# Optimization experiments

Measured on AMD Instinct MI355X. Metric: run time of the kernel, lower is better.

Reference implementation:

```python
import jax, jax.numpy as jnp
import numpy as np

NUM_HEADS = 8  # from init_kwargs
SR = 2         # sr_ratio from init_kwargs


def layernorm(t, g, b, eps=1e-5):
    mu = jnp.mean(t, axis=-1, keepdims=True)
    var = jnp.mean((t - mu) ** 2, axis=-1, keepdims=True)
    return (t - mu) * jax.lax.rsqrt(var + eps) * g + b


def setup_inputs() -> dict:
    key = jax.random.key(0)
    ks = jax.random.split(key, 6)
    B, C = 4, 256
    Hx = Wx = 64
    Hz = Wz = 32
    N = Hz * Wz + Hx * Wx  # 5120 (template tokens first, then search tokens)
    s = 0.02
    return {
        "x": jax.random.normal(ks[0], (B, N, C), jnp.float32),
        "Wq": jax.random.normal(ks[1], (C, C), jnp.float32) * s,          # nn.Linear(dim, dim, bias=False)
        "Wkv": jax.random.normal(ks[2], (2 * C, C), jnp.float32) * s,     # nn.Linear(dim, 2*dim, bias=False)
        "Wsr": jax.random.normal(ks[3], (C, C, SR, SR), jnp.float32) * s, # Conv2d(dim, dim, k=sr, stride=sr) OIHW
        "bsr": jnp.zeros((C,), jnp.float32),
        "gamma": jnp.ones((C,), jnp.float32),
        "beta": jnp.zeros((C,), jnp.float32),
        "Wproj": jax.random.normal(ks[4], (C, C), jnp.float32) * s,
        "bproj": jnp.zeros((C,), jnp.float32),
        "H_x": Hx, "W_x": Wx, "H_z": Hz, "W_z": Wz,
    }


def reference(x, Wq, Wkv, Wsr, bsr, gamma, beta, Wproj, bproj, H_x, W_x, H_z, W_z):
    B, N, C = x.shape
    h = NUM_HEADS
    d = C // h
    scale = d ** -0.5
    Nz, Nx = H_z * W_z, H_x * W_x

    # q for all tokens: [B, h, N, d]
    q = (x @ Wq.T).reshape(B, N, h, d).transpose(0, 2, 1, 3)

    # spatial reduction (sr_ratio > 1 branch): strided conv + layernorm on each stream
    z_tok, x_tok = x[:, :Nz], x[:, Nz:]
    ker = jnp.transpose(Wsr, (2, 3, 1, 0))  # OIHW -> HWIO

    def sr_branch(t, H, W):
        img = t.reshape(B, H, W, C)  # NHWC; same layout as torch NCHW reshape
        out = jax.lax.conv_general_dilated(
            img, ker, window_strides=(SR, SR), padding="VALID",
            dimension_numbers=("NHWC", "HWIO", "NHWC")) + bsr
        out = out.reshape(B, -1, C)
        return layernorm(out, gamma, beta)

    x_ = sr_branch(x_tok, H_x, W_x)  # [B, (Hx/sr)*(Wx/sr), C]
    z_ = sr_branch(z_tok, H_z, W_z)  # [B, (Hz/sr)*(Wz/sr), C]
    zL = z_.shape[1]
    cat = jnp.concatenate([z_, x_], axis=1)  # [B, L, C]

    kv = (cat @ Wkv.T).reshape(B, -1, 2, h, d).transpose(2, 0, 3, 1, 4)  # [2, B, h, L, d]
    k, v = kv[0], kv[1]

    q_z, q_x = q[:, :, :Nz], q[:, :, Nz:]
    k_z, v_z = k[:, :, :zL], v[:, :, :zL]

    # template queries attend only to reduced template keys/values
    attn_z = jax.nn.softmax(jnp.einsum("bhqd,bhkd->bhqk", q_z, k_z) * scale, axis=-1)
    out_z = jnp.einsum("bhqk,bhkd->bhqd", attn_z, v_z).transpose(0, 2, 1, 3).reshape(B, Nz, C)

    # search queries attend to full (template+search) reduced keys/values
    attn_x = jax.nn.softmax(jnp.einsum("bhqd,bhkd->bhqk", q_x, k) * scale, axis=-1)
    out_x = jnp.einsum("bhqk,bhkd->bhqd", attn_x, v).transpose(0, 2, 1, 3).reshape(B, Nx, C)

    out = jnp.concatenate([out_z, out_x], axis=1)
    return out @ Wproj.T + bproj
```

## Files before the change

### kernel.cpp

```cpp
#include <hip/hip_runtime.h>
#include <hip/hip_bf16.h>
#include <cstddef>

#define BATCH 4
#define CCH 256
#define NHEAD 8
#define DHEAD 32
#define NZ 1024
#define NX 4096
#define NTOK 5120
#define LKV 1280
#define QC 0.25503486f

typedef __attribute__((ext_vector_type(8))) short bf16x8;
typedef __attribute__((ext_vector_type(4))) float floatx4;

__device__ inline short f2bf(float f) {
  __hip_bfloat16 h = __float2bfloat16(f);
  return __builtin_bit_cast(short, h);
}
__device__ inline unsigned int pk2(float a, float b) {
  unsigned int lo = (unsigned short)f2bf(a);
  unsigned int hi = (unsigned short)f2bf(b);
  return lo | (hi << 16);
}
__device__ inline unsigned int pk2f(float a, float b) {
  unsigned int ua = __builtin_bit_cast(unsigned int, a) + 0x8000u;
  unsigned int ub = __builtin_bit_cast(unsigned int, b) + 0x8000u;
  return __builtin_amdgcn_perm(ub, ua, 0x07060302u);
}
__device__ inline void cvt8(const float* __restrict__ src, short* __restrict__ dst, int i) {
  float4 v0 = ((const float4*)src)[i * 2];
  float4 v1 = ((const float4*)src)[i * 2 + 1];
  uint4 u;
  u.x = pk2(v0.x, v0.y); u.y = pk2(v0.z, v0.w);
  u.z = pk2(v1.x, v1.y); u.w = pk2(v1.z, v1.w);
  ((uint4*)dst)[i] = u;
}

__global__ __launch_bounds__(256) void prep_weights(const float* __restrict__ Wq,
                                                    const float* __restrict__ Wkv,
                                                    const float* __restrict__ Wproj,
                                                    const float* __restrict__ Wsr,
                                                    const float* __restrict__ x,
                                                    short* __restrict__ Wqb,
                                                    short* __restrict__ Wkvb,
                                                    short* __restrict__ Wprojb,
                                                    short* __restrict__ Wkb,
                                                    short* __restrict__ xb) {
  int blk = blockIdx.x, tid = threadIdx.x;
  if (blk < 32) {
    cvt8(Wq, Wqb, blk * 256 + tid);
  } else if (blk < 96) {
    cvt8(Wkv, Wkvb, (blk - 32) * 256 + tid);
  } else if (blk < 128) {
    cvt8(Wproj, Wprojb, (blk - 96) * 256 + tid);
  } else if (blk < 1152) {
    int i = (blk - 128) * 256 + tid;
    int co = i >> 10;
    int rem = i & 1023;
    int di = rem >> 9, dj = (rem >> 8) & 1, ci = rem & 255;
    Wkb[i] = f2bf(Wsr[((co * 256 + ci) * 2 + di) * 2 + dj]);
  } else {
    cvt8(x, xb, (blk - 1152) * 256 + tid);
  }
}

__global__ __launch_bounds__(256) void im2col_kernel(const float* __restrict__ x,
                                                     short* __restrict__ patch) {
  int blk = blockIdx.x;
  int b = blk / 1280, t = blk % 1280;
  int c = threadIdx.x;
#pragma unroll
  for (int di = 0; di < 2; ++di)
#pragma unroll
    for (int dj = 0; dj < 2; ++dj) {
      int src;
      if (t < 256) {
        int oi = t >> 4, oj = t & 15;
        src = b * NTOK + (2 * oi + di) * 32 + (2 * oj + dj);
      } else {
        int tt = t - 256;
        int oi = tt >> 5, oj = tt & 31;
        src = b * NTOK + NZ + (2 * oi + di) * 64 + (2 * oj + dj);
      }
      patch[(size_t)blk * 1024 + di * 512 + dj * 256 + c] = f2bf(x[(size_t)src * CCH + c]);
    }
}

#define G64_DECL()                                                           \
  __shared__ short As[64][72];                                               \
  __shared__ short Bs[64][72];                                               \
  int tid = threadIdx.x;                                                     \
  int wave = tid >> 6, lg = (tid & 63) >> 4, lr = tid & 15;                  \
  int sr = tid >> 2, sc = tid & 3;                                           \
  floatx4 acc[4] = {{0.f,0.f,0.f,0.f},{0.f,0.f,0.f,0.f},                     \
                    {0.f,0.f,0.f,0.f},{0.f,0.f,0.f,0.f}};

#define G64_MFMA8()                                                          \
    __syncthreads();                                                         \
    {                                                                        \
      bf16x8 af0 = *(bf16x8*)&As[wave * 16 + lr][lg * 8];                    \
      bf16x8 af1 = *(bf16x8*)&As[wave * 16 + lr][32 + lg * 8];               \
      _Pragma("unroll") for (int n = 0; n < 4; ++n) {                        \
        bf16x8 bf0 = *(bf16x8*)&Bs[n * 16 + lr][lg * 8];                     \
        bf16x8 bf1 = *(bf16x8*)&Bs[n * 16 + lr][32 + lg * 8];                \
        acc[n] = __builtin_amdgcn_mfma_f32_16x16x32_bf16(af0, bf0, acc[n], 0, 0, 0); \
        acc[n] = __builtin_amdgcn_mfma_f32_16x16x32_bf16(af1, bf1, acc[n], 0, 0, 0); \
      }                                                                      \
    }

__global__ __launch_bounds__(256) void gemm_qconv(const short* __restrict__ xb,
                                                  const short* __restrict__ Wqb,
                                                  const short* __restrict__ patch,
                                                  const short* __restrict__ Wkb,
                                                  short* __restrict__ qbf,
                                                  float* __restrict__ cat_pre) {
  G64_DECL()
  int bidx = blockIdx.x;
  if (bidx < 1280) {
    int bm = (bidx >> 2) * 64, bn = (bidx & 3) * 64;
    for (int k0 = 0; k0 < 256; k0 += 64) {
      bf16x8 a0 = *(const bf16x8*)&xb[(size_t)(bm + sr) * 256 + k0 + sc * 8];
      bf16x8 a1 = *(const bf16x8*)&xb[(size_t)(bm + sr) * 256 + k0 + (sc + 4) * 8];
      bf16x8 b0 = *(const bf16x8*)&Wqb[(size_t)(bn + sr) * 256 + k0 + sc * 8];
      bf16x8 b1 = *(const bf16x8*)&Wqb[(size_t)(bn + sr) * 256 + k0 + (sc + 4) * 8];
      __syncthreads();
      *(bf16x8*)&As[sr][sc * 8] = a0;
      *(bf16x8*)&As[sr][(sc + 4) * 8] = a1;
      *(bf16x8*)&Bs[sr][sc * 8] = b0;
      *(bf16x8*)&Bs[sr][(sc + 4) * 8] = b1;
      G64_MFMA8()
    }
#pragma unroll
    for (int n = 0; n < 4; ++n) {
      int c = bn + 16 * n + lr;
      int h = c >> 5, d = c & 31;
#pragma unroll
      for (int reg = 0; reg < 4; ++reg) {
        int m = bm + wave * 16 + 4 * lg + reg;
        int b = m / NTOK, tok = m - b * NTOK;
        qbf[((size_t)(b * 8 + h) * NTOK + tok) * 32 + d] = f2bf(acc[n][reg] * QC);
      }
    }
  } else {
    int idx = bidx - 1280;
    int bm = (idx >> 2) * 64, bn = (idx & 3) * 64;
    for (int k0 = 0; k0 < 1024; k0 += 64) {
      bf16x8 a0 = *(const bf16x8*)&patch[(size_t)(bm + sr) * 1024 + k0 + sc * 8];
      bf16x8 a1 = *(const bf16x8*)&patch[(size_t)(bm + sr) * 1024 + k0 + (sc + 4) * 8];
      bf16x8 b0 = *(const bf16x8*)&Wkb[(size_t)(bn + sr) * 1024 + k0 + sc * 8];
      bf16x8 b1 = *(const bf16x8*)&Wkb[(size_t)(bn + sr) * 1024 + k0 + (sc + 4) * 8];
      __syncthreads();
      *(bf16x8*)&As[sr][sc * 8] = a0;
      *(bf16x8*)&As[sr][(sc + 4) * 8] = a1;
      *(bf16x8*)&Bs[sr][sc * 8] = b0;
      *(bf16x8*)&Bs[sr][(sc + 4) * 8] = b1;
      G64_MFMA8()
    }
#pragma unroll
    for (int n = 0; n < 4; ++n) {
      int c = bn + 16 * n + lr;
#pragma unroll
      for (int reg = 0; reg < 4; ++reg) {
        int m = bm + wave * 16 + 4 * lg + reg;
        cat_pre[(size_t)m * 256 + c] = acc[n][reg];
      }
    }
  }
}

__global__ __launch_bounds__(256) void gemm_kv64(const short* __restrict__ A,
                                                 const short* __restrict__ Bm,
                                                 short* __restrict__ Kbf,
                                                 short* __restrict__ Vtb) {
  G64_DECL()
  int bm = blockIdx.y * 64, bn = blockIdx.x * 64;
  for (int k0 = 0; k0 < 256; k0 += 64) {
    bf16x8 a0 = *(const bf16x8*)&A[(size_t)(bm + sr) * 256 + k0 + sc * 8];
    bf16x8 a1 = *(const bf16x8*)&A[(size_t)(bm + sr) * 256 + k0 + (sc + 4) * 8];
    bf16x8 b0 = *(const bf16x8*)&Bm[(size_t)(bn + sr) * 256 + k0 + sc * 8];
    bf16x8 b1 = *(const bf16x8*)&Bm[(size_t)(bn + sr) * 256 + k0 + (sc + 4) * 8];
    __syncthreads();
    *(bf16x8*)&As[sr][sc * 8] = a0;
    *(bf16x8*)&As[sr][(sc + 4) * 8] = a1;
    *(bf16x8*)&Bs[sr][sc * 8] = b0;
    *(bf16x8*)&Bs[sr][(sc + 4) * 8] = b1;
    G64_MFMA8()
  }
#pragma unroll
  for (int n = 0; n < 4; ++n) {
    int c = bn + 16 * n + lr;
#pragma unroll
    for (int reg = 0; reg < 4; ++reg) {
      int m = bm + wave * 16 + 4 * lg + reg;
      int b = m / LKV, kvg = m - b * LKV;
      if (c < 256) {
        int h = c >> 5, d = c & 31;
        Kbf[((size_t)(b * 8 + h) * LKV + kvg) * 32 + d] = f2bf(acc[n][reg]);
      } else {
        int cc = c - 256;
        int h = cc >> 5, d = cc & 31;
        int tile = kvg >> 6, kvin = kvg & 63;
        Vtb[(((size_t)(b * 8 + h) * 20 + tile) * 32 + d) * 64 + kvin] = f2bf(acc[n][reg]);
      }
    }
  }
}

__global__ __launch_bounds__(256) void gemm_proj64(const short* __restrict__ A,
                                                   const short* __restrict__ Bm,
                                                   const float* __restrict__ bias,
                                                   float* __restrict__ Cm) {
  G64_DECL()
  int bm = blockIdx.y * 64, bn = blockIdx.x * 64;
  for (int k0 = 0; k0 < 256; k0 += 64) {
    bf16x8 a0 = *(const bf16x8*)&A[(size_t)(bm + sr) * 256 + k0 + sc * 8];
    bf16x8 a1 = *(const bf16x8*)&A[(size_t)(bm + sr) * 256 + k0 + (sc + 4) * 8];
    bf16x8 b0 = *(const bf16x8*)&Bm[(size_t)(bn + sr) * 256 + k0 + sc * 8];
    bf16x8 b1 = *(const bf16x8*)&Bm[(size_t)(bn + sr) * 256 + k0 + (sc + 4) * 8];
    __syncthreads();
    *(bf16x8*)&As[sr][sc * 8] = a0;
    *(bf16x8*)&As[sr][(sc + 4) * 8] = a1;
    *(bf16x8*)&Bs[sr][sc * 8] = b0;
    *(bf16x8*)&Bs[sr][(sc + 4) * 8] = b1;
    G64_MFMA8()
  }
#pragma unroll
  for (int n = 0; n < 4; ++n) {
    int c = bn + 16 * n + lr;
    float bv = bias[c];
#pragma unroll
    for (int reg = 0; reg < 4; ++reg) {
      int m = bm + wave * 16 + 4 * lg + reg;
      Cm[(size_t)m * 256 + c] = acc[n][reg] + bv;
    }
  }
}

__global__ __launch_bounds__(256) void ln_kernel(const float* __restrict__ cat_pre,
                                                 const float* __restrict__ bsr,
                                                 const float* __restrict__ gamma,
                                                 const float* __restrict__ beta,
                                                 short* __restrict__ catb) {
  int row = blockIdx.x * 4 + (threadIdx.x >> 6);
  int lane = threadIdx.x & 63;
  float4 v = *(const float4*)&cat_pre[(size_t)row * 256 + lane * 4];
  float4 bb = *(const float4*)&bsr[lane * 4];
  v.x += bb.x; v.y += bb.y; v.z += bb.z; v.w += bb.w;
  float s = (v.x + v.y) + (v.z + v.w);
#pragma unroll
  for (int mask = 1; mask < 64; mask <<= 1) s += __shfl_xor(s, mask, 64);
  float mu = s * (1.f / 256.f);
  float4 dv;
  dv.x = v.x - mu; dv.y = v.y - mu; dv.z = v.z - mu; dv.w = v.w - mu;
  float q = dv.x * dv.x + dv.y * dv.y + dv.z * dv.z + dv.w * dv.w;
#pragma unroll
  for (int mask = 1; mask < 64; mask <<= 1) q += __shfl_xor(q, mask, 64);
  float rs = rsqrtf(q * (1.f / 256.f) + 1e-5f);
  float4 g = *(const float4*)&gamma[lane * 4];
  float4 be = *(const float4*)&beta[lane * 4];
  uint2 st;
  st.x = pk2(dv.x * rs * g.x + be.x, dv.y * rs * g.y + be.y);
  st.y = pk2(dv.z * rs * g.z + be.z, dv.w * rs * g.w + be.w);
  *(uint2*)&catb[(size_t)row * 256 + lane * 4] = st;
}

__global__ __launch_bounds__(256) void attn_fused(const short* __restrict__ qbf,
                                                  const short* __restrict__ Kbf,
                                                  const short* __restrict__ Vtb,
                                                  short* __restrict__ attn_out) {
  int blk = blockIdx.x;
  int bh, q0, kvlen;
  if (blk < 512) {
    bh = blk >> 4; q0 = NZ + (blk & 15) * 256; kvlen = LKV;
  } else {
    int idx = blk - 512;
    bh = idx >> 2; q0 = (idx & 3) * 256; kvlen = 256;
  }
  int b = bh >> 3, hh = bh & 7;
  int tid = threadIdx.x;
  int wave = tid >> 6, lane = tid & 63, lg = lane >> 4, lr = lane & 15;

  __shared__ short Ps[4][64][72];

  int qtok = q0 + wave * 64;
  const short* qb = qbf + ((size_t)bh * NTOK + qtok) * 32;
  bf16x8 qf[4];
#pragma unroll
  for (int qi = 0; qi < 4; ++qi)
    qf[qi] = *(const bf16x8*)&qb[(16 * qi + lr) * 32 + lg * 8];

  const short* Kb = Kbf + (size_t)bh * LKV * 32;
  const short* Vb = Vtb + (size_t)bh * 20 * 2048;

  floatx4 oacc[4][2];
#pragma unroll
  for (int qi = 0; qi < 4; ++qi)
#pragma unroll
    for (int n = 0; n < 2; ++n) oacc[qi][n] = (floatx4){0.f, 0.f, 0.f, 0.f};
  float lsum[4] = {0.f, 0.f, 0.f, 0.f};

  bf16x8 kfc[4], vfc[2][2];
#pragma unroll
  for (int m = 0; m < 4; ++m)
    kfc[m] = *(const bf16x8*)&Kb[(size_t)(16 * m + lr) * 32 + lg * 8];
#pragma unroll
  for (int n = 0; n < 2; ++n)
#pragma unroll
    for (int kb = 0; kb < 2; ++kb)
      vfc[n][kb] = *(const bf16x8*)&Vb[(16 * n + lr) * 64 + kb * 32 + lg * 8];

  for (int l0 = 0; l0 < kvlen; l0 += 64) {
    __builtin_amdgcn_sched_barrier(0);
#pragma unroll
    for (int qi = 0; qi < 4; ++qi) {
      floatx4 st[4];
#pragma unroll
      for (int m = 0; m < 4; ++m)
        st[m] = __builtin_amdgcn_mfma_f32_16x16x32_bf16(
            kfc[m], qf[qi], (floatx4){0.f, 0.f, 0.f, 0.f}, 0, 0, 0);
      int pr = 16 * qi + lr;
#pragma unroll
      for (int m = 0; m < 4; ++m) {
        float p0 = __builtin_amdgcn_exp2f(st[m][0]);
        float p1 = __builtin_amdgcn_exp2f(st[m][1]);
        float p2 = __builtin_amdgcn_exp2f(st[m][2]);
        float p3 = __builtin_amdgcn_exp2f(st[m][3]);
        lsum[qi] += (p0 + p1) + (p2 + p3);
        uint2 w;
        w.x = pk2f(p0, p1);
        w.y = pk2f(p2, p3);
        *(uint2*)&Ps[wave][pr][16 * m + 4 * lg] = w;
      }
    }

    bf16x8 kfn[4], vfn[2][2];
    int l1 = l0 + 64;
    if (l1 < kvlen) {
      const short* Vbt = Vb + (l1 >> 6) * 2048;
#pragma unroll
      for (int m = 0; m < 4; ++m)
        kfn[m] = *(const bf16x8*)&Kb[(size_t)(l1 + 16 * m + lr) * 32 + lg * 8];
#pragma unroll
      for (int n = 0; n < 2; ++n)
#pragma unroll
        for (int kb = 0; kb < 2; ++kb)
          vfn[n][kb] = *(const bf16x8*)&Vbt[(16 * n + lr) * 64 + kb * 32 + lg * 8];
    }

    __builtin_amdgcn_sched_barrier(0);

#pragma unroll
    for (int qi = 0; qi < 4; ++qi)
#pragma unroll
      for (int kb = 0; kb < 2; ++kb) {
        bf16x8 pf = *(bf16x8*)&Ps[wave][16 * qi + lr][kb * 32 + lg * 8];
#pragma unroll
        for (int n = 0; n < 2; ++n)
          oacc[qi][n] = __builtin_amdgcn_mfma_f32_16x16x32_bf16(pf, vfc[n][kb], oacc[qi][n], 0, 0, 0);
      }

#pragma unroll
    for (int m = 0; m < 4; ++m) kfc[m] = kfn[m];
#pragma unroll
    for (int n = 0; n < 2; ++n)
#pragma unroll
      for (int kb = 0; kb < 2; ++kb) vfc[n][kb] = vfn[n][kb];
  }

#pragma unroll
  for (int qi = 0; qi < 4; ++qi) {
    lsum[qi] += __shfl_xor(lsum[qi], 16, 64);
    lsum[qi] += __shfl_xor(lsum[qi], 32, 64);
  }

#pragma unroll
  for (int qi = 0; qi < 4; ++qi)
#pragma unroll
    for (int reg = 0; reg < 4; ++reg) {
      float lv = __shfl(lsum[qi], 4 * lg + reg, 64);
      float inv = 1.f / lv;
      int gr = b * NTOK + qtok + 16 * qi + 4 * lg + reg;
      short* ob = attn_out + (size_t)gr * CCH + hh * DHEAD;
      ob[lr]      = f2bf(oacc[qi][0][reg] * inv);
      ob[16 + lr] = f2bf(oacc[qi][1][reg] * inv);
    }
}

extern "C" void kernel_launch(void* const* d_in, const int* in_sizes, int n_in,
                              void* d_out, int out_size, void* d_ws, size_t ws_size,
                              hipStream_t stream) {
  (void)in_sizes; (void)n_in; (void)out_size; (void)ws_size;
  const float* x     = (const float*)d_in[0];
  const float* Wq    = (const float*)d_in[1];
  const float* Wkv   = (const float*)d_in[2];
  const float* Wsr   = (const float*)d_in[3];
  const float* bsr   = (const float*)d_in[4];
  const float* gamma = (const float*)d_in[5];
  const float* beta  = (const float*)d_in[6];
  const float* Wproj = (const float*)d_in[7];
  const float* bproj = (const float*)d_in[8];
  float* out = (float*)d_out;
  float* ws  = (float*)d_ws;

  short* qbf      = (short*)ws;
  short* attn_out = (short*)(ws + 2621440);
  short* patch    = (short*)(ws + 5242880);
  float* cat_pre  = ws + 7864320;
  short* catb     = (short*)(ws + 9175040);
  short* Kbf      = (short*)(ws + 9830400);
  short* Vtb      = (short*)(ws + 10485760);
  short* Wqb      = (short*)(ws + 11141120);
  short* Wkvb     = (short*)(ws + 11173888);
  short* Wkb      = (short*)(ws + 11239424);
  short* Wprojb   = (short*)(ws + 11370496);
  short* xb       = attn_out;

  prep_weights<<<3712, 256, 0, stream>>>(Wq, Wkv, Wproj, Wsr, x, Wqb, Wkvb, Wprojb, Wkb, xb);
  im2col_kernel<<<BATCH * LKV, 256, 0, stream>>>(x, patch);
  gemm_qconv<<<1600, 256, 0, stream>>>(xb, Wqb, patch, Wkb, qbf, cat_pre);
  ln_kernel<<<1280, 256, 0, stream>>>(cat_pre, bsr, gamma, beta, catb);
  gemm_kv64<<<dim3(8, 80), 256, 0, stream>>>(catb, Wkvb, Kbf, Vtb);
  attn_fused<<<640, 256, 0, stream>>>(qbf, Kbf, Vtb, attn_out);
  gemm_proj64<<<dim3(4, 320), 256, 0, stream>>>(attn_out, Wprojb, bproj, out);
}
```

Before: 189.0 us.

## Fuse im2col into conv GEMM, swizzle attention blocks, prioritize MFMA waves

Drops the separate im2col kernel. The strided-conv GEMM now gathers its A operand directly from the bf16 copy of x by computing the source token row for each k-chunk, which removes a launch and the write and re-read of the patch buffer. The attention kernel remaps block indices so long-KV and short-KV blocks are interleaved across the grid, and it raises wave priority around the MFMA sections with s_setprio. In exchange, the gathered loads in the conv GEMM are less regular and the prio hints may not help scheduling.

```diff
diff --git a/kernel.cpp b/kernel.cpp
--- a/kernel.cpp
+++ b/kernel.cpp
@@ -66,28 +66,6 @@
   }
 }
 
-__global__ __launch_bounds__(256) void im2col_kernel(const float* __restrict__ x,
-                                                     short* __restrict__ patch) {
-  int blk = blockIdx.x;
-  int b = blk / 1280, t = blk % 1280;
-  int c = threadIdx.x;
-#pragma unroll
-  for (int di = 0; di < 2; ++di)
-#pragma unroll
-    for (int dj = 0; dj < 2; ++dj) {
-      int src;
-      if (t < 256) {
-        int oi = t >> 4, oj = t & 15;
-        src = b * NTOK + (2 * oi + di) * 32 + (2 * oj + dj);
-      } else {
-        int tt = t - 256;
-        int oi = tt >> 5, oj = tt & 31;
-        src = b * NTOK + NZ + (2 * oi + di) * 64 + (2 * oj + dj);
-      }
-      patch[(size_t)blk * 1024 + di * 512 + dj * 256 + c] = f2bf(x[(size_t)src * CCH + c]);
-    }
-}
-
 #define G64_DECL()                                                           \
   __shared__ short As[64][72];                                               \
   __shared__ short Bs[64][72];                                               \
@@ -112,7 +90,6 @@
 
 __global__ __launch_bounds__(256) void gemm_qconv(const short* __restrict__ xb,
                                                   const short* __restrict__ Wqb,
-                                                  const short* __restrict__ patch,
                                                   const short* __restrict__ Wkb,
                                                   short* __restrict__ qbf,
                                                   float* __restrict__ cat_pre) {
@@ -145,10 +122,24 @@
     }
   } else {
     int idx = bidx - 1280;
-    int bm = (idx >> 2) * 64, bn = (idx & 3) * 64;
+    int mt = idx >> 2;
+    int bm = mt * 64, bn = (idx & 3) * 64;
+    int bq = mt / 20;
+    int tloc = (mt % 20) * 64 + sr;
     for (int k0 = 0; k0 < 1024; k0 += 64) {
-      bf16x8 a0 = *(const bf16x8*)&patch[(size_t)(bm + sr) * 1024 + k0 + sc * 8];
-      bf16x8 a1 = *(const bf16x8*)&patch[(size_t)(bm + sr) * 1024 + k0 + (sc + 4) * 8];
+      int di = k0 >> 9, dj = (k0 >> 8) & 1;
+      int srow;
+      if (tloc < 256) {
+        int oi = tloc >> 4, oj = tloc & 15;
+        srow = bq * NTOK + (2 * oi + di) * 32 + (2 * oj + dj);
+      } else {
+        int tt = tloc - 256;
+        int oi = tt >> 5, oj = tt & 31;
+        srow = bq * NTOK + NZ + (2 * oi + di) * 64 + (2 * oj + dj);
+      }
+      int cb = k0 & 255;
+      bf16x8 a0 = *(const bf16x8*)&xb[(size_t)srow * 256 + cb + sc * 8];
+      bf16x8 a1 = *(const bf16x8*)&xb[(size_t)srow * 256 + cb + (sc + 4) * 8];
       bf16x8 b0 = *(const bf16x8*)&Wkb[(size_t)(bn + sr) * 1024 + k0 + sc * 8];
       bf16x8 b1 = *(const bf16x8*)&Wkb[(size_t)(bn + sr) * 1024 + k0 + (sc + 4) * 8];
       __syncthreads();
@@ -270,7 +261,8 @@
                                                   const short* __restrict__ Kbf,
                                                   const short* __restrict__ Vtb,
                                                   short* __restrict__ attn_out) {
-  int blk = blockIdx.x;
+  int orig = blockIdx.x;
+  int blk = (orig & 7) * 80 + (orig >> 3);
   int bh, q0, kvlen;
   if (blk < 512) {
     bh = blk >> 4; q0 = NZ + (blk & 15) * 256; kvlen = LKV;
@@ -316,10 +308,12 @@
 #pragma unroll
     for (int qi = 0; qi < 4; ++qi) {
       floatx4 st[4];
+      __builtin_amdgcn_s_setprio(1);
 #pragma unroll
       for (int m = 0; m < 4; ++m)
         st[m] = __builtin_amdgcn_mfma_f32_16x16x32_bf16(
             kfc[m], qf[qi], (floatx4){0.f, 0.f, 0.f, 0.f}, 0, 0, 0);
+      __builtin_amdgcn_s_setprio(0);
       int pr = 16 * qi + lr;
 #pragma unroll
       for (int m = 0; m < 4; ++m) {
@@ -351,6 +345,7 @@
 
     __builtin_amdgcn_sched_barrier(0);
 
+    __builtin_amdgcn_s_setprio(1);
 #pragma unroll
     for (int qi = 0; qi < 4; ++qi)
 #pragma unroll
@@ -360,6 +355,7 @@
         for (int n = 0; n < 2; ++n)
           oacc[qi][n] = __builtin_amdgcn_mfma_f32_16x16x32_bf16(pf, vfc[n][kb], oacc[qi][n], 0, 0, 0);
       }
+    __builtin_amdgcn_s_setprio(0);
 
 #pragma unroll
     for (int m = 0; m < 4; ++m) kfc[m] = kfn[m];
@@ -406,7 +402,6 @@
 
   short* qbf      = (short*)ws;
   short* attn_out = (short*)(ws + 2621440);
-  short* patch    = (short*)(ws + 5242880);
   float* cat_pre  = ws + 7864320;
   short* catb     = (short*)(ws + 9175040);
   short* Kbf      = (short*)(ws + 9830400);
@@ -418,8 +413,7 @@
   short* xb       = attn_out;
 
   prep_weights<<<3712, 256, 0, stream>>>(Wq, Wkv, Wproj, Wsr, x, Wqb, Wkvb, Wprojb, Wkb, xb);
-  im2col_kernel<<<BATCH * LKV, 256, 0, stream>>>(x, patch);
-  gemm_qconv<<<1600, 256, 0, stream>>>(xb, Wqb, patch, Wkb, qbf, cat_pre);
+  gemm_qconv<<<1600, 256, 0, stream>>>(xb, Wqb, Wkb, qbf, cat_pre);
   ln_kernel<<<1280, 256, 0, stream>>>(cat_pre, bsr, gamma, beta, catb);
   gemm_kv64<<<dim3(8, 80), 256, 0, stream>>>(catb, Wkvb, Kbf, Vtb);
   attn_fused<<<640, 256, 0, stream>>>(qbf, Kbf, Vtb, attn_out);
```

Result: slower. 210.6 us (+11.4%).
